# Performance work log

Hardware: AMD Instinct MI355X
Metric: run time of the kernel (lower is better)

Reference implementation:

```python
import jax, jax.numpy as jnp
import numpy as np

S, G, NMUL, LENF = 730, 4000, 2, 15
NEARZERO = 1e-5

# param bounds (change_param_range: lb + raw*(ub-lb)), raw in [0,1]
HBV_LB = np.array([1., 50., .05, .01, .001, .2, 0., 0., -2.5, .5, 0., 0.], np.float32)
HBV_UB = np.array([6., 1000., .9, .5, .2, 1., 10., 100., 2.5, 10., .1, .2], np.float32)
EXP_LB = np.array([0., 100., 10., 0., 0., -3.], np.float32)
EXP_UB = np.array([.1, 1500., 50., 5., 3., 0.], np.float32)


def _descale(raw, lb, ub):
    # raw: [G, n_par, NMUL]
    return lb[None, :, None] + raw * (ub - lb)[None, :, None]


def _hbv(P, T, PET, ph):
    # ph: [G,12,NMUL]; order: beta fc k0 k1 k2 lp perc uzl tt cfmax cfr cwh
    beta, fc, k0, k1, k2, lp, perc, uzl, tt, cfmax, cfr, cwh = [ph[:, i, :] for i in range(12)]

    def step(carry, inp):
        sp, mw, sm, suz, slz = carry
        p, t, pet = inp
        rain = jnp.where(t >= tt, p, 0.)
        sp = sp + jnp.where(t < tt, p, 0.)
        melt = jnp.minimum(jnp.maximum(cfmax * (t - tt), 0.), sp)
        mw = mw + melt; sp = sp - melt
        refr = jnp.minimum(jnp.maximum(cfr * cfmax * (tt - t), 0.), mw)
        sp = sp + refr; mw = mw - refr
        tosoil = jnp.maximum(mw - cwh * sp, 0.)
        mw = mw - tosoil
        sw = jnp.clip((sm / fc) ** beta, 0., 1.)
        rech = (rain + tosoil) * sw
        sm = sm + rain + tosoil - rech
        excess = jnp.maximum(sm - fc, 0.); sm = sm - excess
        et = jnp.minimum(pet * jnp.clip(sm / (lp * fc), 0., 1.), sm)
        sm = jnp.maximum(sm - et, NEARZERO)
        suz = suz + rech + excess
        pa = jnp.minimum(perc, suz); suz = suz - pa
        q0 = k0 * jnp.maximum(suz - uzl, 0.); suz = suz - q0
        q1 = k1 * suz; suz = suz - q1
        slz = slz + pa
        q2 = k2 * slz; slz = slz - q2
        return (sp, mw, sm, suz, slz), q0 + q1 + q2

    z = jnp.full_like(fc, NEARZERO)
    init = (z, z, 0.5 * fc, z, z)
    _, q = jax.lax.scan(step, init, (P, T, PET))
    return q  # [S,G,NMUL]


def _exphydro(P, T, PET, pe):
    # pe: [G,6,NMUL]; order: f smax qmax df tmax tmin
    f, smax, qmax, df, tmax, tmin = [pe[:, i, :] for i in range(6)]

    def step(carry, inp):
        s0, s1 = carry
        p, t, pet = inp
        ps = jnp.where(t <= tmin, p, 0.)
        pr = p - ps
        melt = jnp.where(t > tmax, jnp.minimum(s0, df * (t - tmax)), 0.)
        s0 = s0 + ps - melt
        s1 = s1 + pr + melt
        qspill = jnp.maximum(s1 - smax, 0.); s1 = s1 - qspill
        et = jnp.minimum(pet * jnp.clip(s1 / smax, 0., 1.), s1); s1 = s1 - et
        qb = jnp.minimum(qmax * jnp.exp(-f * jnp.maximum(smax - s1, 0.)), s1)
        s1 = s1 - qb
        return (s0, s1), qspill + qb

    z = jnp.full_like(smax, NEARZERO)
    init = (z, 0.5 * smax)
    _, q = jax.lax.scan(step, init, (P, T, PET))
    return q  # [S,G,NMUL]


def _uh_gamma(a, b):
    # a,b: [G]; gamma-pdf unit hydrograph, lenF=LENF
    aa = jax.nn.relu(a) + 0.1
    th = jax.nn.relu(b) + 0.5
    t = jnp.arange(LENF, dtype=jnp.float32) + 0.5  # [LENF]
    logw = (-jax.scipy.special.gammaln(aa)[None, :] - aa[None, :] * jnp.log(th)[None, :]
            + (aa - 1.)[None, :] * jnp.log(t)[:, None] - t[:, None] / th[None, :])
    w = jnp.exp(logw)
    return w / w.sum(0, keepdims=True)  # [LENF,G]


def _route(q, w):
    # causal depthwise conv: out[t,g] = sum_k w[k,g] * q[t-k,g]
    qp = jnp.pad(q, ((LENF - 1, 0), (0, 0)))
    out = jnp.zeros_like(q)
    for k in range(LENF):
        out = out + w[k][None, :] * qp[LENF - 1 - k: LENF - 1 - k + q.shape[0]]
    return out


def setup_inputs() -> dict:
    key = jax.random.key(0)
    k1, k2 = jax.random.split(key)
    u = jax.random.uniform(k1, (S, G, 3), dtype=jnp.float32)
    # physical forcing ranges: prcp [0,10] mm/d, tmean [-10,20] C, pet [0,5] mm/d
    x = jnp.stack([u[..., 0] * 10., u[..., 1] * 30. - 10., u[..., 2] * 5.], axis=-1)
    raw_phy_static = jax.random.uniform(k2, (G, 18 * NMUL + 2), dtype=jnp.float32)
    return {"x": x, "raw_phy_static": raw_phy_static}


def reference(x, raw_phy_static):
    # unpack: [G, 18*NMUL] static block + 2 routing params
    static = raw_phy_static[:, :18 * NMUL].reshape(G, 18, NMUL)
    ph = _descale(static[:, :12, :], jnp.asarray(HBV_LB), jnp.asarray(HBV_UB))
    pe = _descale(static[:, 12:, :], jnp.asarray(EXP_LB), jnp.asarray(EXP_UB))
    route = raw_phy_static[:, 18 * NMUL:]
    rout_a = route[:, 0] * 2.9   # bounds [0, 2.9]
    rout_b = route[:, 1] * 6.5   # bounds [0, 6.5]

    P = jnp.broadcast_to(x[:, :, 0, None], (S, G, NMUL))
    T = jnp.broadcast_to(x[:, :, 1, None], (S, G, NMUL))
    PET = jnp.broadcast_to(x[:, :, 2, None], (S, G, NMUL))

    q_hbv = _hbv(P, T, PET, ph)
    q_exp = _exphydro(P, T, PET, pe)
    qsim = 0.5 * (q_hbv.mean(-1) + q_exp.mean(-1))  # blend over models, mean over nmul -> [S,G]

    w = _uh_gamma(rout_a, rout_b)
    return _route(qsim, w)  # [S,G] routed streamflow
```

## Files before the change

### kernel.cpp

```cpp
#include <hip/hip_runtime.h>

#define SS 730
#define GG 4000
#define LENF 15
#define PD 10
#define GPAD 4032
#define TT 73
#define QN ((size_t)SS * GG)
#define QNI ((int)(SS * GG))

template<bool STORE4>
__global__ __launch_bounds__(64, 1) void hydro_scan(const float* __restrict__ x,
                                                    const float* __restrict__ raw,
                                                    float* __restrict__ qsim) {
    int tid = blockIdx.x * 64 + threadIdx.x;
    int g = tid % GPAD;
    int inst = tid / GPAD;
    if (g >= GG) return;
    int m = inst & 1;
    const float* pr = raw + (size_t)g * 38 + m;

    int xoff = g * 3;
    int qoff = g + (STORE4 ? inst * QNI : 0);

    float pb[PD], tb[PD], eb[PD];
#pragma unroll
    for (int j = 0; j < PD; ++j) {
        pb[j] = x[xoff]; tb[j] = x[xoff + 1]; eb[j] = x[xoff + 2];
        xoff += 3 * GG;
    }

    if (inst < 2) {
        float beta  = 1.0f   + pr[0]  * 5.0f;
        float fc    = 50.0f  + pr[2]  * 950.0f;
        float k0    = 0.05f  + pr[4]  * 0.85f;
        float k1    = 0.01f  + pr[6]  * 0.49f;
        float k2    = 0.001f + pr[8]  * 0.199f;
        float lp    = 0.2f   + pr[10] * 0.8f;
        float perc  =          pr[12] * 10.0f;
        float uzl   =          pr[14] * 100.0f;
        float tt    = -2.5f  + pr[16] * 5.0f;
        float cfmax = 0.5f   + pr[18] * 9.5f;
        float cfr   =          pr[20] * 0.1f;
        float cwh   =          pr[22] * 0.2f;
        float invfc   = 1.0f / fc;
        float invlpfc = 1.0f / (lp * fc);
        float ncfrcf  = -(cfr * cfmax);
        float omk0    = 1.0f - k0;
        float k0uzl   = k0 * uzl;
        float omk1    = 1.0f - k1;

        float sp = 1e-5f, mw = 1e-5f, sm = 0.5f * fc, suz = 1e-5f, slz = 1e-5f;

        auto body = [&](float p, float tc, float pet) -> float {
            float dt   = tc - tt;
            float msn  = fmaxf(cfmax * dt, 0.0f);
            float mrf  = fmaxf(ncfrcf * dt, 0.0f);
            float rain = (dt >= 0.0f) ? p : 0.0f;
            float snow = p - rain;
            float etk  = fmaf(-invlpfc, pet, 1.0f);
            float sw   = exp2f(beta * __log2f(sm * invfc));
            float omsw = 1.0f - sw;
            float sp1  = sp + snow;
            float melt = fminf(msn, sp1);
            float mw2  = mw + melt;
            float sp2  = sp1 - melt;
            float refr = fminf(mrf, mw2);
            float mw3  = mw2 - refr;
            sp = sp2 + refr;
            float mw4  = fminf(mw3, cwh * sp);
            float tosoil = mw3 - mw4;
            mw = mw4;
            float rt    = rain + tosoil;
            float sm1   = fmaf(rt, omsw, sm);
            float rech  = rt * sw;
            float excess = fmaxf(sm1 - fc, 0.0f);
            float sm2   = fminf(sm1, fc);
            sm = fmaxf(fmaxf(sm2 * etk, sm2 - pet), 1e-5f);
            float suz1 = suz + rech + excess;
            float suz2 = fmaxf(suz1 - perc, 0.0f);
            float pa   = suz1 - suz2;
            float suz3 = fminf(suz2, fmaf(suz2, omk0, k0uzl));
            float suzn = omk1 * suz3;
            float q01  = suz2 - suzn;
            suz = suzn;
            float slz1 = slz + pa;
            float q2   = k2 * slz1;
            slz = slz1 - q2;
            return q01 + q2;
        };

        for (int c = 0; c < SS / PD - 1; ++c) {
#pragma unroll
            for (int j = 0; j < PD; ++j) {
                float p = pb[j], tc = tb[j], pet = eb[j];
                pb[j] = x[xoff]; tb[j] = x[xoff + 1]; eb[j] = x[xoff + 2];
                xoff += 3 * GG;
                float q = body(p, tc, pet);
                if (STORE4) qsim[qoff] = q; else atomicAdd(&qsim[qoff], 0.25f * q);
                qoff += GG;
            }
        }
#pragma unroll
        for (int j = 0; j < PD; ++j) {
            float q = body(pb[j], tb[j], eb[j]);
            if (STORE4) qsim[qoff] = q; else atomicAdd(&qsim[qoff], 0.25f * q);
            qoff += GG;
        }
    } else {
        const float* pe = pr + 24;
        float f    =           pe[0]  * 0.1f;
        float smax = 100.0f  + pe[2]  * 1400.0f;
        float qmax = 10.0f   + pe[4]  * 40.0f;
        float df   =           pe[6]  * 5.0f;
        float tmax =           pe[8]  * 3.0f;
        float tmin = -3.0f   + pe[10] * 3.0f;
        float invsmax = 1.0f / smax;
        float fl = f * 1.44269504f;
        float c0 = __log2f(qmax) - fl * smax;

        float s0 = 1e-5f, s1 = 0.5f * smax;

        auto body = [&](float p, float tc, float pet) -> float {
            float mdf = df * fmaxf(tc - tmax, 0.0f);
            float ps  = (tc <= tmin) ? p : 0.0f;
            float prr = p - ps;
            float etk = fmaxf(fmaf(-invsmax, pet, 1.0f), 0.0f);
            float mlt = fminf(s0, mdf);
            s0 = fmaxf(s0 - mdf, 0.0f) + ps;
            float s1a = s1 + prr + mlt;
            float qspill = fmaxf(s1a - smax, 0.0f);
            float s1b = fminf(s1a, smax);
            float s1c = s1b * etk;
            float qb  = fminf(exp2f(fmaf(fl, s1c, c0)), s1c);
            s1 = s1c - qb;
            return qspill + qb;
        };

        for (int c = 0; c < SS / PD - 1; ++c) {
#pragma unroll
            for (int j = 0; j < PD; ++j) {
                float p = pb[j], tc = tb[j], pet = eb[j];
                pb[j] = x[xoff]; tb[j] = x[xoff + 1]; eb[j] = x[xoff + 2];
                xoff += 3 * GG;
                float q = body(p, tc, pet);
                if (STORE4) qsim[qoff] = q; else atomicAdd(&qsim[qoff], 0.25f * q);
                qoff += GG;
            }
        }
#pragma unroll
        for (int j = 0; j < PD; ++j) {
            float q = body(pb[j], tb[j], eb[j]);
            if (STORE4) qsim[qoff] = q; else atomicAdd(&qsim[qoff], 0.25f * q);
            qoff += GG;
        }
    }
}

__global__ __launch_bounds__(256) void uh_weights(const float* __restrict__ raw,
                                                  float* __restrict__ wbuf) {
    int g = blockIdx.x * 256 + threadIdx.x;
    if (g >= GG) return;
    float a = raw[(size_t)g * 38 + 36] * 2.9f;
    float b = raw[(size_t)g * 38 + 37] * 6.5f;
    float aa = fmaxf(a, 0.0f) + 0.1f;
    float th = fmaxf(b, 0.0f) + 0.5f;
    float am1 = aa - 1.0f;
    float invth = 1.0f / th;

    const float logt[LENF] = {
        -0.69314718f, 0.40546511f, 0.91629073f, 1.25276297f, 1.50407740f,
         1.70474809f, 1.87180218f, 2.01490302f, 2.14006616f, 2.25129180f,
         2.35137526f, 2.44234704f, 2.52572864f, 2.60268969f, 2.67414865f };

    float w[LENF];
    float s = 0.0f;
#pragma unroll
    for (int k = 0; k < LENF; ++k) {
        float tk = (float)k + 0.5f;
        w[k] = expf(am1 * logt[k] - tk * invth);
        s += w[k];
    }
    float scale = 0.25f / s;
#pragma unroll
    for (int k = 0; k < LENF; ++k)
        wbuf[(size_t)k * GG + g] = w[k] * scale;
}

template<int NB, bool WPRE>
__global__ __launch_bounds__(256) void hydro_route(const float* __restrict__ qsim,
                                                   const float* __restrict__ raw,
                                                   const float* __restrict__ wbuf,
                                                   float* __restrict__ out) {
    int idx = blockIdx.x * 256 + threadIdx.x;
    if (idx >= GG * (SS / TT)) return;
    int g = idx % GG;
    int c = idx / GG;
    int t0 = c * TT;

    float w[LENF];
    float scale;
    if (WPRE) {
#pragma unroll
        for (int k = 0; k < LENF; ++k)
            w[k] = wbuf[(size_t)k * GG + g];
        scale = 1.0f;
    } else {
        float a = raw[(size_t)g * 38 + 36] * 2.9f;
        float b = raw[(size_t)g * 38 + 37] * 6.5f;
        float aa = fmaxf(a, 0.0f) + 0.1f;
        float th = fmaxf(b, 0.0f) + 0.5f;
        float am1 = aa - 1.0f;
        float invth = 1.0f / th;
        const float logt[LENF] = {
            -0.69314718f, 0.40546511f, 0.91629073f, 1.25276297f, 1.50407740f,
             1.70474809f, 1.87180218f, 2.01490302f, 2.14006616f, 2.25129180f,
             2.35137526f, 2.44234704f, 2.52572864f, 2.60268969f, 2.67414865f };
        float s = 0.0f;
#pragma unroll
        for (int k = 0; k < LENF; ++k) {
            float tk = (float)k + 0.5f;
            w[k] = expf(am1 * logt[k] - tk * invth);
            s += w[k];
        }
        scale = (NB == 4 ? 0.25f : 1.0f) / s;
    }

    float v[TT + LENF - 1];
#pragma unroll
    for (int i = 0; i < TT + LENF - 1; ++i) {
        int tp = t0 - (LENF - 1) + i;
        float sv = 0.0f;
        if (tp >= 0) {
            const float* qb = qsim + (size_t)tp * GG + g;
            sv = qb[0];
            if (NB == 4) sv += qb[QN] + qb[2 * QN] + qb[3 * QN];
        }
        v[i] = sv;
    }
#pragma unroll
    for (int j = 0; j < TT; ++j) {
        float acc = 0.0f;
#pragma unroll
        for (int k = 0; k < LENF; ++k)
            acc += w[k] * v[j + (LENF - 1) - k];
        out[(size_t)(t0 + j) * GG + g] = (WPRE ? acc : acc * scale);
    }
}

extern "C" void kernel_launch(void* const* d_in, const int* in_sizes, int n_in,
                              void* d_out, int out_size, void* d_ws, size_t ws_size,
                              hipStream_t stream) {
    const float* x   = (const float*)d_in[0];
    const float* raw = (const float*)d_in[1];
    float* out  = (float*)d_out;
    float* qsim = (float*)d_ws;

    const size_t slices4 = 4 * QN * sizeof(float);
    const size_t wbytes  = (size_t)LENF * GG * sizeof(float);
    int rblocks = (GG * (SS / TT) + 255) / 256;
    int sblocks = (4 * GPAD) / 64;

    if (ws_size >= slices4 + wbytes) {
        float* wbuf = qsim + 4 * QN;
        hydro_scan<true><<<sblocks, 64, 0, stream>>>(x, raw, qsim);
        uh_weights<<<(GG + 255) / 256, 256, 0, stream>>>(raw, wbuf);
        hydro_route<4, true><<<rblocks, 256, 0, stream>>>(qsim, raw, wbuf, out);
    } else {
        hipMemsetAsync(qsim, 0, QN * sizeof(float), stream);
        hydro_scan<false><<<sblocks, 64, 0, stream>>>(x, raw, qsim);
        hydro_route<1, false><<<rblocks, 256, 0, stream>>>(qsim, raw, nullptr, out);
    }
}
```

Measured before the change: 128.0 us.

## Fuse unit-hydrograph routing into scan kernel via ring-buffer accumulators

Each scan thread computes its own gamma unit-hydrograph weights and applies the routing convolution incrementally with a 15-entry rotating register accumulator. It writes already-routed partial outputs per instance, and a small float4 kernel then sums the four slices into the output. This drops the separate weight and routing kernels and the re-read of the four qsim slices with their 14-step halo. In exchange the scan loop does about 15 extra FMAs per step and holds more registers, and it is unrolled 30-wide to keep the ring-buffer indices static.

```diff
diff --git a/kernel.cpp b/kernel.cpp
--- a/kernel.cpp
+++ b/kernel.cpp
@@ -5,11 +5,11 @@
 #define LENF 15
 #define PD 10
 #define GPAD 4032
-#define TT 73
+#define TT 10
 #define QN ((size_t)SS * GG)
 #define QNI ((int)(SS * GG))
 
-template<bool STORE4>
+template<bool FUSED>
 __global__ __launch_bounds__(64, 1) void hydro_scan(const float* __restrict__ x,
                                                     const float* __restrict__ raw,
                                                     float* __restrict__ qsim) {
@@ -21,7 +21,34 @@
     const float* pr = raw + (size_t)g * 38 + m;
 
     int xoff = g * 3;
-    int qoff = g + (STORE4 ? inst * QNI : 0);
+    int qoff = g + (FUSED ? inst * QNI : 0);
+
+    float w[LENF];
+    if (FUSED) {
+        const float logt[LENF] = {
+            -0.69314718f, 0.40546511f, 0.91629073f, 1.25276297f, 1.50407740f,
+             1.70474809f, 1.87180218f, 2.01490302f, 2.14006616f, 2.25129180f,
+             2.35137526f, 2.44234704f, 2.52572864f, 2.60268969f, 2.67414865f };
+        float a = raw[(size_t)g * 38 + 36] * 2.9f;
+        float b = raw[(size_t)g * 38 + 37] * 6.5f;
+        float aa = fmaxf(a, 0.0f) + 0.1f;
+        float th = fmaxf(b, 0.0f) + 0.5f;
+        float am1 = aa - 1.0f;
+        float invth = 1.0f / th;
+        float s = 0.0f;
+#pragma unroll
+        for (int k = 0; k < LENF; ++k) {
+            float tk = (float)k + 0.5f;
+            w[k] = expf(am1 * logt[k] - tk * invth);
+            s += w[k];
+        }
+        float ws = 0.25f / s;
+#pragma unroll
+        for (int k = 0; k < LENF; ++k) w[k] *= ws;
+    }
+    float racc[LENF];
+#pragma unroll
+    for (int k = 0; k < LENF; ++k) racc[k] = 0.0f;
 
     float pb[PD], tb[PD], eb[PD];
 #pragma unroll
@@ -29,6 +56,16 @@
         pb[j] = x[xoff]; tb[j] = x[xoff + 1]; eb[j] = x[xoff + 2];
         xoff += 3 * GG;
     }
+
+    auto route_tail = [&](float q, int s) {
+        float o = fmaf(w[0], q, racc[s]);
+        qsim[qoff] = o;
+        qoff += GG;
+        racc[s] = 0.0f;
+#pragma unroll
+        for (int k = 1; k < LENF; ++k)
+            racc[(s + k) % LENF] = fmaf(w[k], q, racc[(s + k) % LENF]);
+    };
 
     if (inst < 2) {
         float beta  = 1.0f   + pr[0]  * 5.0f;
@@ -90,22 +127,36 @@
             return q01 + q2;
         };
 
-        for (int c = 0; c < SS / PD - 1; ++c) {
+        if (FUSED) {
+            for (int cc = 0; cc < 24; ++cc) {
+#pragma unroll
+                for (int j2 = 0; j2 < 30; ++j2) {
+                    const int j = j2 % PD;
+                    float p = pb[j], tc = tb[j], pet = eb[j];
+                    pb[j] = x[xoff]; tb[j] = x[xoff + 1]; eb[j] = x[xoff + 2];
+                    xoff += 3 * GG;
+                    route_tail(body(p, tc, pet), j2 % LENF);
+                }
+            }
+#pragma unroll
+            for (int j = 0; j < PD; ++j)
+                route_tail(body(pb[j], tb[j], eb[j]), j % LENF);
+        } else {
+            for (int c = 0; c < SS / PD - 1; ++c) {
+#pragma unroll
+                for (int j = 0; j < PD; ++j) {
+                    float p = pb[j], tc = tb[j], pet = eb[j];
+                    pb[j] = x[xoff]; tb[j] = x[xoff + 1]; eb[j] = x[xoff + 2];
+                    xoff += 3 * GG;
+                    atomicAdd(&qsim[qoff], 0.25f * body(p, tc, pet));
+                    qoff += GG;
+                }
+            }
 #pragma unroll
             for (int j = 0; j < PD; ++j) {
-                float p = pb[j], tc = tb[j], pet = eb[j];
-                pb[j] = x[xoff]; tb[j] = x[xoff + 1]; eb[j] = x[xoff + 2];
-                xoff += 3 * GG;
-                float q = body(p, tc, pet);
-                if (STORE4) qsim[qoff] = q; else atomicAdd(&qsim[qoff], 0.25f * q);
+                atomicAdd(&qsim[qoff], 0.25f * body(pb[j], tb[j], eb[j]));
                 qoff += GG;
             }
-        }
-#pragma unroll
-        for (int j = 0; j < PD; ++j) {
-            float q = body(pb[j], tb[j], eb[j]);
-            if (STORE4) qsim[qoff] = q; else atomicAdd(&qsim[qoff], 0.25f * q);
-            qoff += GG;
         }
     } else {
         const float* pe = pr + 24;
@@ -137,42 +188,76 @@
             return qspill + qb;
         };
 
-        for (int c = 0; c < SS / PD - 1; ++c) {
+        if (FUSED) {
+            for (int cc = 0; cc < 24; ++cc) {
+#pragma unroll
+                for (int j2 = 0; j2 < 30; ++j2) {
+                    const int j = j2 % PD;
+                    float p = pb[j], tc = tb[j], pet = eb[j];
+                    pb[j] = x[xoff]; tb[j] = x[xoff + 1]; eb[j] = x[xoff + 2];
+                    xoff += 3 * GG;
+                    route_tail(body(p, tc, pet), j2 % LENF);
+                }
+            }
+#pragma unroll
+            for (int j = 0; j < PD; ++j)
+                route_tail(body(pb[j], tb[j], eb[j]), j % LENF);
+        } else {
+            for (int c = 0; c < SS / PD - 1; ++c) {
+#pragma unroll
+                for (int j = 0; j < PD; ++j) {
+                    float p = pb[j], tc = tb[j], pet = eb[j];
+                    pb[j] = x[xoff]; tb[j] = x[xoff + 1]; eb[j] = x[xoff + 2];
+                    xoff += 3 * GG;
+                    atomicAdd(&qsim[qoff], 0.25f * body(p, tc, pet));
+                    qoff += GG;
+                }
+            }
 #pragma unroll
             for (int j = 0; j < PD; ++j) {
-                float p = pb[j], tc = tb[j], pet = eb[j];
-                pb[j] = x[xoff]; tb[j] = x[xoff + 1]; eb[j] = x[xoff + 2];
-                xoff += 3 * GG;
-                float q = body(p, tc, pet);
-                if (STORE4) qsim[qoff] = q; else atomicAdd(&qsim[qoff], 0.25f * q);
+                atomicAdd(&qsim[qoff], 0.25f * body(pb[j], tb[j], eb[j]));
                 qoff += GG;
             }
         }
-#pragma unroll
-        for (int j = 0; j < PD; ++j) {
-            float q = body(pb[j], tb[j], eb[j]);
-            if (STORE4) qsim[qoff] = q; else atomicAdd(&qsim[qoff], 0.25f * q);
-            qoff += GG;
-        }
     }
 }
 
-__global__ __launch_bounds__(256) void uh_weights(const float* __restrict__ raw,
-                                                  float* __restrict__ wbuf) {
-    int g = blockIdx.x * 256 + threadIdx.x;
-    if (g >= GG) return;
+__global__ __launch_bounds__(256) void sum4(const float* __restrict__ r,
+                                            float* __restrict__ out) {
+    int i = blockIdx.x * 256 + threadIdx.x;
+    if (i >= (int)(QN / 4)) return;
+    const float4* r0 = (const float4*)r;
+    const float4* r1 = (const float4*)(r + QN);
+    const float4* r2 = (const float4*)(r + 2 * QN);
+    const float4* r3 = (const float4*)(r + 3 * QN);
+    float4 a = r0[i], b = r1[i], c = r2[i], d = r3[i];
+    float4 o;
+    o.x = (a.x + b.x) + (c.x + d.x);
+    o.y = (a.y + b.y) + (c.y + d.y);
+    o.z = (a.z + b.z) + (c.z + d.z);
+    o.w = (a.w + b.w) + (c.w + d.w);
+    ((float4*)out)[i] = o;
+}
+
+__global__ __launch_bounds__(256) void hydro_route1(const float* __restrict__ qsim,
+                                                    const float* __restrict__ raw,
+                                                    float* __restrict__ out) {
+    int idx = blockIdx.x * 256 + threadIdx.x;
+    if (idx >= GG * (SS / TT)) return;
+    int g = idx % GG;
+    int c = idx / GG;
+    int t0 = c * TT;
+
     float a = raw[(size_t)g * 38 + 36] * 2.9f;
     float b = raw[(size_t)g * 38 + 37] * 6.5f;
     float aa = fmaxf(a, 0.0f) + 0.1f;
     float th = fmaxf(b, 0.0f) + 0.5f;
     float am1 = aa - 1.0f;
     float invth = 1.0f / th;
-
     const float logt[LENF] = {
         -0.69314718f, 0.40546511f, 0.91629073f, 1.25276297f, 1.50407740f,
          1.70474809f, 1.87180218f, 2.01490302f, 2.14006616f, 2.25129180f,
          2.35137526f, 2.44234704f, 2.52572864f, 2.60268969f, 2.67414865f };
-
     float w[LENF];
     float s = 0.0f;
 #pragma unroll
@@ -181,62 +266,13 @@
         w[k] = expf(am1 * logt[k] - tk * invth);
         s += w[k];
     }
-    float scale = 0.25f / s;
-#pragma unroll
-    for (int k = 0; k < LENF; ++k)
-        wbuf[(size_t)k * GG + g] = w[k] * scale;
-}
-
-template<int NB, bool WPRE>
-__global__ __launch_bounds__(256) void hydro_route(const float* __restrict__ qsim,
-                                                   const float* __restrict__ raw,
-                                                   const float* __restrict__ wbuf,
-                                                   float* __restrict__ out) {
-    int idx = blockIdx.x * 256 + threadIdx.x;
-    if (idx >= GG * (SS / TT)) return;
-    int g = idx % GG;
-    int c = idx / GG;
-    int t0 = c * TT;
-
-    float w[LENF];
-    float scale;
-    if (WPRE) {
-#pragma unroll
-        for (int k = 0; k < LENF; ++k)
-            w[k] = wbuf[(size_t)k * GG + g];
-        scale = 1.0f;
-    } else {
-        float a = raw[(size_t)g * 38 + 36] * 2.9f;
-        float b = raw[(size_t)g * 38 + 37] * 6.5f;
-        float aa = fmaxf(a, 0.0f) + 0.1f;
-        float th = fmaxf(b, 0.0f) + 0.5f;
-        float am1 = aa - 1.0f;
-        float invth = 1.0f / th;
-        const float logt[LENF] = {
-            -0.69314718f, 0.40546511f, 0.91629073f, 1.25276297f, 1.50407740f,
-             1.70474809f, 1.87180218f, 2.01490302f, 2.14006616f, 2.25129180f,
-             2.35137526f, 2.44234704f, 2.52572864f, 2.60268969f, 2.67414865f };
-        float s = 0.0f;
-#pragma unroll
-        for (int k = 0; k < LENF; ++k) {
-            float tk = (float)k + 0.5f;
-            w[k] = expf(am1 * logt[k] - tk * invth);
-            s += w[k];
-        }
-        scale = (NB == 4 ? 0.25f : 1.0f) / s;
-    }
+    float scale = 1.0f / s;
 
     float v[TT + LENF - 1];
 #pragma unroll
     for (int i = 0; i < TT + LENF - 1; ++i) {
         int tp = t0 - (LENF - 1) + i;
-        float sv = 0.0f;
-        if (tp >= 0) {
-            const float* qb = qsim + (size_t)tp * GG + g;
-            sv = qb[0];
-            if (NB == 4) sv += qb[QN] + qb[2 * QN] + qb[3 * QN];
-        }
-        v[i] = sv;
+        v[i] = (tp >= 0) ? qsim[(size_t)tp * GG + g] : 0.0f;
     }
 #pragma unroll
     for (int j = 0; j < TT; ++j) {
@@ -244,7 +280,7 @@
 #pragma unroll
         for (int k = 0; k < LENF; ++k)
             acc += w[k] * v[j + (LENF - 1) - k];
-        out[(size_t)(t0 + j) * GG + g] = (WPRE ? acc : acc * scale);
+        out[(size_t)(t0 + j) * GG + g] = acc * scale;
     }
 }
 
@@ -257,18 +293,14 @@
     float* qsim = (float*)d_ws;
 
     const size_t slices4 = 4 * QN * sizeof(float);
-    const size_t wbytes  = (size_t)LENF * GG * sizeof(float);
-    int rblocks = (GG * (SS / TT) + 255) / 256;
     int sblocks = (4 * GPAD) / 64;
 
-    if (ws_size >= slices4 + wbytes) {
-        float* wbuf = qsim + 4 * QN;
+    if (ws_size >= slices4) {
         hydro_scan<true><<<sblocks, 64, 0, stream>>>(x, raw, qsim);
-        uh_weights<<<(GG + 255) / 256, 256, 0, stream>>>(raw, wbuf);
-        hydro_route<4, true><<<rblocks, 256, 0, stream>>>(qsim, raw, wbuf, out);
+        sum4<<<((int)(QN / 4) + 255) / 256, 256, 0, stream>>>(qsim, out);
     } else {
         hipMemsetAsync(qsim, 0, QN * sizeof(float), stream);
         hydro_scan<false><<<sblocks, 64, 0, stream>>>(x, raw, qsim);
-        hydro_route<1, false><<<rblocks, 256, 0, stream>>>(qsim, raw, nullptr, out);
+        hydro_route1<<<(GG * (SS / TT) + 255) / 256, 256, 0, stream>>>(qsim, raw, out);
     }
 }
```

Result: faster. 124.1 us (-3.1%).

## Fuse UH weight computation into LDS-staged routing kernel, drop weights kernel

Applied to the files above, without the earlier changes.

Removes the separate uh_weights kernel and its global weight buffer by computing the gamma unit-hydrograph weights inside the routing kernel. The routing kernel now stages the summed four qsim slices for a 128-gauge by 87-step window in shared memory. The convolution then reads from LDS rather than holding a large per-thread register array. This saves a kernel launch and a global round trip, and lowers register pressure. The cost is an extra __syncthreads and LDS traffic, and each block recomputes the exp-based weights.

```diff
diff --git a/kernel.cpp b/kernel.cpp
--- a/kernel.cpp
+++ b/kernel.cpp
@@ -5,7 +5,10 @@
 #define LENF 15
 #define PD 10
 #define GPAD 4032
-#define TT 73
+#define TT 10
+#define RTT 73
+#define RG 128
+#define NGT ((GG + RG - 1) / RG)
 #define QN ((size_t)SS * GG)
 #define QNI ((int)(SS * GG))
 
@@ -157,22 +160,42 @@
     }
 }
 
-__global__ __launch_bounds__(256) void uh_weights(const float* __restrict__ raw,
-                                                  float* __restrict__ wbuf) {
-    int g = blockIdx.x * 256 + threadIdx.x;
-    if (g >= GG) return;
+__global__ __launch_bounds__(RG) void hydro_route_lds(const float* __restrict__ qsim,
+                                                      const float* __restrict__ raw,
+                                                      float* __restrict__ out) {
+    __shared__ float lds[RTT + LENF - 1][RG];
+
+    int gt = blockIdx.x % NGT;
+    int bt = blockIdx.x / NGT;
+    int g0 = gt * RG;
+    int t0 = bt * RTT;
+    int tl = threadIdx.x;
+    int g  = g0 + tl;
+
+    bool gok = (g < GG);
+#pragma unroll 4
+    for (int r = 0; r < RTT + LENF - 1; ++r) {
+        int tp = t0 - (LENF - 1) + r;
+        float v = 0.0f;
+        if (tp >= 0 && gok) {
+            const float* qb = qsim + (size_t)tp * GG + g;
+            v = (qb[0] + qb[QN]) + (qb[2 * QN] + qb[3 * QN]);
+        }
+        lds[r][tl] = v;
+    }
+    __syncthreads();
+    if (!gok) return;
+
+    const float logt[LENF] = {
+        -0.69314718f, 0.40546511f, 0.91629073f, 1.25276297f, 1.50407740f,
+         1.70474809f, 1.87180218f, 2.01490302f, 2.14006616f, 2.25129180f,
+         2.35137526f, 2.44234704f, 2.52572864f, 2.60268969f, 2.67414865f };
     float a = raw[(size_t)g * 38 + 36] * 2.9f;
     float b = raw[(size_t)g * 38 + 37] * 6.5f;
     float aa = fmaxf(a, 0.0f) + 0.1f;
     float th = fmaxf(b, 0.0f) + 0.5f;
     float am1 = aa - 1.0f;
     float invth = 1.0f / th;
-
-    const float logt[LENF] = {
-        -0.69314718f, 0.40546511f, 0.91629073f, 1.25276297f, 1.50407740f,
-         1.70474809f, 1.87180218f, 2.01490302f, 2.14006616f, 2.25129180f,
-         2.35137526f, 2.44234704f, 2.52572864f, 2.60268969f, 2.67414865f };
-
     float w[LENF];
     float s = 0.0f;
 #pragma unroll
@@ -181,62 +204,53 @@
         w[k] = expf(am1 * logt[k] - tk * invth);
         s += w[k];
     }
-    float scale = 0.25f / s;
-#pragma unroll
-    for (int k = 0; k < LENF; ++k)
-        wbuf[(size_t)k * GG + g] = w[k] * scale;
-}
-
-template<int NB, bool WPRE>
-__global__ __launch_bounds__(256) void hydro_route(const float* __restrict__ qsim,
-                                                   const float* __restrict__ raw,
-                                                   const float* __restrict__ wbuf,
-                                                   float* __restrict__ out) {
+    float ws = 0.25f / s;
+#pragma unroll
+    for (int k = 0; k < LENF; ++k) w[k] *= ws;
+
+    for (int j = 0; j < RTT; ++j) {
+        float acc = 0.0f;
+#pragma unroll
+        for (int k = 0; k < LENF; ++k)
+            acc = fmaf(w[k], lds[j + (LENF - 1) - k][tl], acc);
+        out[(size_t)(t0 + j) * GG + g] = acc;
+    }
+}
+
+__global__ __launch_bounds__(256) void hydro_route1(const float* __restrict__ qsim,
+                                                    const float* __restrict__ raw,
+                                                    float* __restrict__ out) {
     int idx = blockIdx.x * 256 + threadIdx.x;
     if (idx >= GG * (SS / TT)) return;
     int g = idx % GG;
     int c = idx / GG;
     int t0 = c * TT;
 
+    float a = raw[(size_t)g * 38 + 36] * 2.9f;
+    float b = raw[(size_t)g * 38 + 37] * 6.5f;
+    float aa = fmaxf(a, 0.0f) + 0.1f;
+    float th = fmaxf(b, 0.0f) + 0.5f;
+    float am1 = aa - 1.0f;
+    float invth = 1.0f / th;
+    const float logt[LENF] = {
+        -0.69314718f, 0.40546511f, 0.91629073f, 1.25276297f, 1.50407740f,
+         1.70474809f, 1.87180218f, 2.01490302f, 2.14006616f, 2.25129180f,
+         2.35137526f, 2.44234704f, 2.52572864f, 2.60268969f, 2.67414865f };
     float w[LENF];
-    float scale;
-    if (WPRE) {
-#pragma unroll
-        for (int k = 0; k < LENF; ++k)
-            w[k] = wbuf[(size_t)k * GG + g];
-        scale = 1.0f;
-    } else {
-        float a = raw[(size_t)g * 38 + 36] * 2.9f;
-        float b = raw[(size_t)g * 38 + 37] * 6.5f;
-        float aa = fmaxf(a, 0.0f) + 0.1f;
-        float th = fmaxf(b, 0.0f) + 0.5f;
-        float am1 = aa - 1.0f;
-        float invth = 1.0f / th;
-        const float logt[LENF] = {
-            -0.69314718f, 0.40546511f, 0.91629073f, 1.25276297f, 1.50407740f,
-             1.70474809f, 1.87180218f, 2.01490302f, 2.14006616f, 2.25129180f,
-             2.35137526f, 2.44234704f, 2.52572864f, 2.60268969f, 2.67414865f };
-        float s = 0.0f;
-#pragma unroll
-        for (int k = 0; k < LENF; ++k) {
-            float tk = (float)k + 0.5f;
-            w[k] = expf(am1 * logt[k] - tk * invth);
-            s += w[k];
-        }
-        scale = (NB == 4 ? 0.25f : 1.0f) / s;
-    }
+    float s = 0.0f;
+#pragma unroll
+    for (int k = 0; k < LENF; ++k) {
+        float tk = (float)k + 0.5f;
+        w[k] = expf(am1 * logt[k] - tk * invth);
+        s += w[k];
+    }
+    float scale = 1.0f / s;
 
     float v[TT + LENF - 1];
 #pragma unroll
     for (int i = 0; i < TT + LENF - 1; ++i) {
         int tp = t0 - (LENF - 1) + i;
-        float sv = 0.0f;
-        if (tp >= 0) {
-            const float* qb = qsim + (size_t)tp * GG + g;
-            sv = qb[0];
-            if (NB == 4) sv += qb[QN] + qb[2 * QN] + qb[3 * QN];
-        }
-        v[i] = sv;
+        v[i] = (tp >= 0) ? qsim[(size_t)tp * GG + g] : 0.0f;
     }
 #pragma unroll
     for (int j = 0; j < TT; ++j) {
@@ -244,7 +258,7 @@
 #pragma unroll
         for (int k = 0; k < LENF; ++k)
             acc += w[k] * v[j + (LENF - 1) - k];
-        out[(size_t)(t0 + j) * GG + g] = (WPRE ? acc : acc * scale);
+        out[(size_t)(t0 + j) * GG + g] = acc * scale;
     }
 }
 
@@ -257,18 +271,14 @@
     float* qsim = (float*)d_ws;
 
     const size_t slices4 = 4 * QN * sizeof(float);
-    const size_t wbytes  = (size_t)LENF * GG * sizeof(float);
-    int rblocks = (GG * (SS / TT) + 255) / 256;
     int sblocks = (4 * GPAD) / 64;
 
-    if (ws_size >= slices4 + wbytes) {
-        float* wbuf = qsim + 4 * QN;
+    if (ws_size >= slices4) {
         hydro_scan<true><<<sblocks, 64, 0, stream>>>(x, raw, qsim);
-        uh_weights<<<(GG + 255) / 256, 256, 0, stream>>>(raw, wbuf);
-        hydro_route<4, true><<<rblocks, 256, 0, stream>>>(qsim, raw, wbuf, out);
+        hydro_route_lds<<<NGT * (SS / RTT), RG, 0, stream>>>(qsim, raw, out);
     } else {
         hipMemsetAsync(qsim, 0, QN * sizeof(float), stream);
         hydro_scan<false><<<sblocks, 64, 0, stream>>>(x, raw, qsim);
-        hydro_route<1, false><<<rblocks, 256, 0, stream>>>(qsim, raw, nullptr, out);
-    }
-}
+        hydro_route1<<<(GG * (SS / TT) + 255) / 256, 256, 0, stream>>>(qsim, raw, out);
+    }
+}
```

Result: no change. 130.2 us (+1.7%).
